# Kernel optimization log

Hardware: AMD Instinct MI355X
Metric: run time of the kernel (lower is better)

Reference implementation:

```python
import jax, jax.numpy as jnp
import numpy as np

EPS = 1e-5

def layer_norm(h, g, b):
    m = h.mean(-1, keepdims=True)
    v = ((h - m) ** 2).mean(-1, keepdims=True)
    return (h - m) * jax.lax.rsqrt(v + EPS) * g + b

def setup_inputs() -> dict:
    key = jax.random.key(0)
    ks = jax.random.split(key, 16)
    B, D, C, H, EH, L = 64, 20000, 16, 64, 128, 32
    s = lambda k, fan_in, shape: jax.random.normal(k, shape, jnp.float32) / np.sqrt(fan_in)
    return {
        "x": jax.random.normal(ks[0], (B, D), jnp.float32),
        "mask": jax.random.randint(ks[1], (B, D), 0, 2, jnp.int32),
        "feature_embedding": jax.random.normal(ks[2], (D, C), jnp.float32),
        # h_layer: Linear(1+C -> H), LN, ReLU, Linear(H -> C), LN, ReLU
        "W1": s(ks[3], 1 + C, (1 + C, H)), "b1": jnp.zeros((H,), jnp.float32),
        "g1": jnp.ones((H,), jnp.float32), "be1": jnp.zeros((H,), jnp.float32),
        "W2": s(ks[4], H, (H, C)), "b2": jnp.zeros((C,), jnp.float32),
        "g2": jnp.ones((C,), jnp.float32), "be2": jnp.zeros((C,), jnp.float32),
        # encoder_mlp (FCLayers, 2 layers, LayerNorm + ReLU each): C -> EH -> 2L
        "We1": s(ks[5], C, (C, EH)), "bb1": jnp.zeros((EH,), jnp.float32),
        "gg1": jnp.ones((EH,), jnp.float32), "bbe1": jnp.zeros((EH,), jnp.float32),
        "We2": s(ks[6], EH, (EH, 2 * L)), "bb2": jnp.zeros((2 * L,), jnp.float32),
        "gg2": jnp.ones((2 * L,), jnp.float32), "bbe2": jnp.zeros((2 * L,), jnp.float32),
    }

def reference(x, mask, feature_embedding, W1, b1, g1, be1, W2, b2, g2, be2,
              We1, bb1, gg1, bbe1, We2, bb2, gg2, bbe2):
    B, D = x.shape
    C = feature_embedding.shape[1]
    # per-feature point-net: h_layer runs row-wise, so we compute it densely
    # for all (b, d) and zero out unobserved entries before pooling —
    # identical math to the per-sample masked gather in the original.
    h_in = jnp.concatenate(
        [x[..., None], jnp.broadcast_to(feature_embedding, (B, D, C))], axis=-1
    )  # [B, D, 1+C]
    h = jax.nn.relu(layer_norm(h_in @ W1 + b1, g1, be1))   # [B, D, H]
    h = jax.nn.relu(layer_norm(h @ W2 + b2, g2, be2))      # [B, D, C]
    m = mask.astype(h.dtype)
    summed = jnp.einsum('bdc,bd->bc', h, m)                # masked sum pool
    num_obs = jnp.maximum(m.sum(axis=1, keepdims=True), 1.0)
    c = summed / num_obs                                   # pool_mode='mean'
    # encoder_mlp
    e = jax.nn.relu(layer_norm(c @ We1 + bb1, gg1, bbe1))
    e = jax.nn.relu(layer_norm(e @ We2 + bb2, gg2, bbe2))  # [B, 2*latent]
    mu, logvar = jnp.split(e, 2, axis=-1)
    return mu, logvar
```

## Files before the change

### kernel.cpp

```cpp
#include <hip/hip_runtime.h>
#include <hip/hip_bf16.h>

#define EPSF 1e-5f

namespace {
constexpr int B = 64, D = 20000, C = 16, H = 64, EH = 128, L = 32;
constexpr int CHUNK = 256;
constexpr int GX = 26;
constexpr int PB = 16;
}

typedef __attribute__((ext_vector_type(8))) short bf16x8;
typedef __attribute__((ext_vector_type(4))) float f32x4;

static __device__ __forceinline__ unsigned short f2bf(float f) {
    __hip_bfloat16 h = __float2bfloat16(f);
    return __builtin_bit_cast(unsigned short, h);
}
static __device__ __forceinline__ unsigned int packbf(float lo, float hi) {
    return ((unsigned int)f2bf(hi) << 16) | (unsigned int)f2bf(lo);
}

__global__ __launch_bounds__(1024) void k_prep(
    const int* __restrict__ mask, const float* __restrict__ fe,
    const float* __restrict__ W1, const float* __restrict__ b1,
    const float* __restrict__ W2,
    unsigned short* __restrict__ cd, int* __restrict__ cnt,
    unsigned short* __restrict__ febf,
    unsigned short* __restrict__ W1T, unsigned short* __restrict__ W2T)
{
    const int t = threadIdx.x;
    if (blockIdx.x < B) {
        const int b = blockIdx.x;
        const int lane = t & 63, wid = t >> 6;
        __shared__ int wc[16];
        const size_t bD = (size_t)b * D;
        constexpr int NIT = (D + 1023) / 1024;
        int mv = (t < D) ? mask[bD + t] : 0;
        int base = 0;
        for (int it = 0; it < NIT; ++it) {
            int mv_next = 0;
            const int dn = (it + 1) * 1024 + t;
            if (it + 1 < NIT && dn < D) mv_next = mask[bD + dn];
            const unsigned long long bal = __ballot(mv != 0);
            if (lane == 0) wc[wid] = __popcll(bal);
            __syncthreads();
            int woff = 0, tot = 0;
            #pragma unroll
            for (int k2 = 0; k2 < 16; ++k2) {
                const int c0 = wc[k2];
                tot += c0;
                if (k2 < wid) woff += c0;
            }
            if (mv) {
                const int d = it * 1024 + t;
                const int pre = __popcll(bal & ((1ull << lane) - 1ull));
                cd[bD + base + woff + pre] = (unsigned short)d;
            }
            base += tot;
            __syncthreads();
            mv = mv_next;
        }
        if (t == 0) cnt[b] = base;
    } else {
        const int pb = blockIdx.x - B;
        const int gtid = pb * 1024 + t;
        for (int u = gtid; u < (D * C) / 8; u += PB * 1024) {
            const float4 f0 = *(const float4*)(fe + (size_t)u * 8);
            const float4 f1 = *(const float4*)(fe + (size_t)u * 8 + 4);
            uint4 pk;
            pk.x = packbf(f0.x, f0.y); pk.y = packbf(f0.z, f0.w);
            pk.z = packbf(f1.x, f1.y); pk.w = packbf(f1.z, f1.w);
            *(uint4*)(febf + (size_t)u * 8) = pk;
        }
        if (pb == 0) {
            for (int e = t; e < H * 32; e += 1024) {
                const int h = e >> 5, kk = e & 31;
                float v = 0.f;
                if (kk < 16)       v = W1[(kk + 1) * H + h];
                else if (kk == 16) v = W1[h];
                else if (kk == 17) v = b1[h];
                W1T[e] = f2bf(v);
            }
        } else if (pb == 1) {
            for (int e = t; e < C * H; e += 1024) {
                const int c0 = e >> 6, hh = e & 63;
                W2T[e] = f2bf(W2[hh * C + c0]);
            }
        }
    }
}

__global__ __launch_bounds__(256, 4) void k_rows(
    const float* __restrict__ x, const unsigned short* __restrict__ cd,
    const int* __restrict__ cnt, const unsigned short* __restrict__ febf,
    const unsigned short* __restrict__ W1T, const unsigned short* __restrict__ W2T,
    const float* __restrict__ g1, const float* __restrict__ be1,
    const float* __restrict__ g2, const float* __restrict__ be2,
    const float* __restrict__ b2,
    float* __restrict__ part)
{
    const int b  = blockIdx.y;
    const int bx = blockIdx.x;
    const int n  = cnt[b];
    const int tid = threadIdx.x;
    const int w = tid >> 6, lane = tid & 63;
    const int g = lane >> 4, q = lane & 15;
    const size_t bD = (size_t)b * D;

    bf16x8 w1f[4];
    #pragma unroll
    for (int m = 0; m < 4; ++m)
        w1f[m] = *(const bf16x8*)(W1T + (16 * m + q) * 32 + 8 * g);
    bf16x8 w2f[2];
    #pragma unroll
    for (int ks = 0; ks < 2; ++ks)
        w2f[ks] = *(const bf16x8*)(W2T + q * 64 + 32 * ks + 8 * g);

    float4 g1v[4], be1v[4];
    #pragma unroll
    for (int m = 0; m < 4; ++m) {
        g1v[m]  = *(const float4*)(g1  + 16 * m + 4 * g);
        be1v[m] = *(const float4*)(be1 + 16 * m + 4 * g);
    }
    const float4 g2v  = *(const float4*)(g2  + 4 * g);
    const float4 be2v = *(const float4*)(be2 + 4 * g);
    const float4 b2v  = *(const float4*)(b2  + 4 * g);

    __shared__ __align__(16) unsigned short Rs[4][4][8][16][8];
    __shared__ float wsum[4][16];

    f32x4 acc = {0.f, 0.f, 0.f, 0.f};

    const int nch = (n + CHUNK - 1) / CHUNK;
    for (int j = bx; j < nch; j += GX) {
        const int cbase = j * CHUNK + w * 64;

        bf16x8 hb[4];
        #pragma unroll
        for (int it = 0; it < 4; ++it) {
            const int gb = cbase + it * 16;
            bf16x8 hv;
            #pragma unroll
            for (int e = 0; e < 8; ++e) hv[e] = 0;
            if (gb < n) {
                const int idx = gb + q;
                const bool v = idx < n;
                if (g < 2) {
                    int d = 0;
                    if (v) d = cd[bD + idx];
                    hv = *(const bf16x8*)(febf + (size_t)d * 16 + 8 * g);
                } else if (g == 2) {
                    float xv = 0.f;
                    if (v) { const int d = cd[bD + idx]; xv = x[bD + d]; }
                    hv[0] = (short)f2bf(xv);
                    hv[1] = (short)0x3F80;
                }
            }
            hb[it] = hv;
        }

        #pragma unroll
        for (int it = 0; it < 4; ++it) {
            const int gb = cbase + it * 16;
            if (gb >= n) continue;
            const f32x4 z = {0.f, 0.f, 0.f, 0.f};
            f32x4 t1a[4];
            #pragma unroll
            for (int m = 0; m < 4; ++m)
                t1a[m] = __builtin_amdgcn_mfma_f32_16x16x32_bf16(w1f[m], hb[it], z, 0, 0, 0);

            float s0 = 0.f, s1 = 0.f, q0 = 0.f, q1 = 0.f;
            #pragma unroll
            for (int m = 0; m < 4; ++m) {
                s0 += t1a[m][0] + t1a[m][1];
                s1 += t1a[m][2] + t1a[m][3];
                q0 = fmaf(t1a[m][0], t1a[m][0], fmaf(t1a[m][1], t1a[m][1], q0));
                q1 = fmaf(t1a[m][2], t1a[m][2], fmaf(t1a[m][3], t1a[m][3], q1));
            }
            float s = s0 + s1, sq = q0 + q1;
            s  += __shfl_xor(s, 16);  sq += __shfl_xor(sq, 16);
            s  += __shfl_xor(s, 32);  sq += __shfl_xor(sq, 32);
            const float mean1 = s * (1.f / H);
            const float var1  = fmaxf(sq * (1.f / H) - mean1 * mean1, 0.f);
            const float rstd1 = rsqrtf(var1 + EPSF);

            #pragma unroll
            for (int m = 0; m < 4; ++m) {
                const float v0 = fmaxf(fmaf((t1a[m][0] - mean1) * rstd1, g1v[m].x, be1v[m].x), 0.f);
                const float v1 = fmaxf(fmaf((t1a[m][1] - mean1) * rstd1, g1v[m].y, be1v[m].y), 0.f);
                const float v2 = fmaxf(fmaf((t1a[m][2] - mean1) * rstd1, g1v[m].z, be1v[m].z), 0.f);
                const float v3 = fmaxf(fmaf((t1a[m][3] - mean1) * rstd1, g1v[m].w, be1v[m].w), 0.f);
                uint2 pk = make_uint2(packbf(v0, v1), packbf(v2, v3));
                *(uint2*)&Rs[w][it][2 * m + (g >> 1)][q][4 * (g & 1)] = pk;
            }

            const bf16x8 rb0 = *(const bf16x8*)&Rs[w][it][g][q][0];
            const bf16x8 rb1 = *(const bf16x8*)&Rs[w][it][4 + g][q][0];
            f32x4 a2 = __builtin_amdgcn_mfma_f32_16x16x32_bf16(w2f[0], rb0, z, 0, 0, 0);
            a2 = __builtin_amdgcn_mfma_f32_16x16x32_bf16(w2f[1], rb1, a2, 0, 0, 0);
            a2[0] += b2v.x; a2[1] += b2v.y; a2[2] += b2v.z; a2[3] += b2v.w;

            float s2 = (a2[0] + a2[1]) + (a2[2] + a2[3]);
            float q2 = fmaf(a2[0], a2[0], fmaf(a2[1], a2[1],
                       fmaf(a2[2], a2[2], a2[3] * a2[3])));
            s2 += __shfl_xor(s2, 16);  q2 += __shfl_xor(q2, 16);
            s2 += __shfl_xor(s2, 32);  q2 += __shfl_xor(q2, 32);
            const float mean2 = s2 * (1.f / C);
            const float var2  = fmaxf(q2 * (1.f / C) - mean2 * mean2, 0.f);
            const float rstd2 = rsqrtf(var2 + EPSF);
            const float vm = (gb + q < n) ? 1.f : 0.f;
            acc[0] += fmaxf(fmaf((a2[0] - mean2) * rstd2, g2v.x, be2v.x), 0.f) * vm;
            acc[1] += fmaxf(fmaf((a2[1] - mean2) * rstd2, g2v.y, be2v.y), 0.f) * vm;
            acc[2] += fmaxf(fmaf((a2[2] - mean2) * rstd2, g2v.z, be2v.z), 0.f) * vm;
            acc[3] += fmaxf(fmaf((a2[3] - mean2) * rstd2, g2v.w, be2v.w), 0.f) * vm;
        }
    }

    #pragma unroll
    for (int off = 1; off < 16; off <<= 1) {
        #pragma unroll
        for (int r = 0; r < 4; ++r) acc[r] += __shfl_xor(acc[r], off);
    }
    if (q == 0)
        *(float4*)&wsum[w][4 * g] = make_float4(acc[0], acc[1], acc[2], acc[3]);
    __syncthreads();
    if (tid < C)
        part[((size_t)b * GX + bx) * C + tid] =
            wsum[0][tid] + wsum[1][tid] + wsum[2][tid] + wsum[3][tid];
}

__global__ __launch_bounds__(EH) void k_enc(
    const float* __restrict__ part, const int* __restrict__ cnt,
    const float* __restrict__ We1, const float* __restrict__ bb1,
    const float* __restrict__ gg1, const float* __restrict__ bbe1,
    const float* __restrict__ We2, const float* __restrict__ bb2,
    const float* __restrict__ gg2, const float* __restrict__ bbe2,
    float* __restrict__ out)
{
    const int b = blockIdx.x;
    const int t = threadIdx.x;
    __shared__ float cc[C];
    __shared__ float stats[2];
    __shared__ float buf[EH];
    __shared__ float buf2[2 * L];

    const int n = cnt[b];
    if (t < C) {
        float s = 0.f;
        #pragma unroll
        for (int j = 0; j < GX; ++j)
            s += part[((size_t)b * GX + j) * C + t];
        cc[t] = s;
    }
    __syncthreads();
    const float inv = 1.f / fmaxf((float)n, 1.f);

    float v1 = bb1[t];
    #pragma unroll
    for (int c = 0; c < C; ++c)
        v1 = fmaf(cc[c] * inv, We1[c * EH + t], v1);
    buf[t] = v1;
    __syncthreads();
    if (t == 0) {
        float s = 0.f, ss = 0.f;
        for (int j2 = 0; j2 < EH; ++j2) { s += buf[j2]; ss = fmaf(buf[j2], buf[j2], ss); }
        float mn = s * (1.f / EH);
        float vr = fmaxf(ss * (1.f / EH) - mn * mn, 0.f);
        stats[0] = mn; stats[1] = rsqrtf(vr + EPSF);
    }
    __syncthreads();
    float e1 = fmaxf(fmaf((v1 - stats[0]) * stats[1], gg1[t], bbe1[t]), 0.f);
    __syncthreads();
    buf[t] = e1;
    __syncthreads();

    float v2 = 0.f;
    if (t < 2 * L) {
        v2 = bb2[t];
        #pragma unroll
        for (int h = 0; h < EH; ++h)
            v2 = fmaf(buf[h], We2[h * (2 * L) + t], v2);
        buf2[t] = v2;
    }
    __syncthreads();
    if (t == 0) {
        float s = 0.f, ss = 0.f;
        for (int j2 = 0; j2 < 2 * L; ++j2) { s += buf2[j2]; ss = fmaf(buf2[j2], buf2[j2], ss); }
        float mn = s * (1.f / (2 * L));
        float vr = fmaxf(ss * (1.f / (2 * L)) - mn * mn, 0.f);
        stats[0] = mn; stats[1] = rsqrtf(vr + EPSF);
    }
    __syncthreads();
    if (t < 2 * L) {
        float e2 = fmaxf(fmaf((v2 - stats[0]) * stats[1], gg2[t], bbe2[t]), 0.f);
        if (t < L) out[(size_t)b * L + t]                       = e2;
        else       out[(size_t)B * L + (size_t)b * L + (t - L)] = e2;
    }
}

extern "C" void kernel_launch(void* const* d_in, const int* in_sizes, int n_in,
                              void* d_out, int out_size, void* d_ws, size_t ws_size,
                              hipStream_t stream) {
    const float* x    = (const float*)d_in[0];
    const int*   mask = (const int*)d_in[1];
    const float* fe   = (const float*)d_in[2];
    const float* W1   = (const float*)d_in[3];
    const float* b1   = (const float*)d_in[4];
    const float* g1   = (const float*)d_in[5];
    const float* be1  = (const float*)d_in[6];
    const float* W2   = (const float*)d_in[7];
    const float* b2   = (const float*)d_in[8];
    const float* g2   = (const float*)d_in[9];
    const float* be2  = (const float*)d_in[10];
    const float* We1  = (const float*)d_in[11];
    const float* bb1  = (const float*)d_in[12];
    const float* gg1  = (const float*)d_in[13];
    const float* bbe1 = (const float*)d_in[14];
    const float* We2  = (const float*)d_in[15];
    const float* bb2  = (const float*)d_in[16];
    const float* gg2  = (const float*)d_in[17];
    const float* bbe2 = (const float*)d_in[18];
    float* out = (float*)d_out;

    char* wp = (char*)d_ws;
    float* part     = (float*)wp;               wp += (size_t)B * GX * C * 4;
    int*   cnt      = (int*)wp;                 wp += (size_t)B * 4;
    unsigned short* W1T  = (unsigned short*)wp; wp += (size_t)H * 32 * 2;
    unsigned short* W2T  = (unsigned short*)wp; wp += (size_t)C * H * 2;
    unsigned short* febf = (unsigned short*)wp; wp += (size_t)D * C * 2;
    unsigned short* cd   = (unsigned short*)wp;

    hipLaunchKernelGGL(k_prep, dim3(B + PB), dim3(1024), 0, stream,
                       mask, fe, W1, b1, W2, cd, cnt, febf, W1T, W2T);
    hipLaunchKernelGGL(k_rows, dim3(GX, B), dim3(256), 0, stream,
                       x, cd, cnt, febf, W1T, W2T, g1, be1, g2, be2, b2, part);
    hipLaunchKernelGGL(k_enc, dim3(B), dim3(EH), 0, stream,
                       part, cnt, We1, bb1, gg1, bbe1, We2, bb2, gg2, bbe2, out);
}
```

Measured before the change: 54.73 us.

## Flatten row work into global 64-row units and pass layer-1 output in registers

The row kernel stops using a fixed grid of 26 blocks per batch. Each wave now takes a global 64-element unit found through a prefix sum of per-batch unit counts, which balances load across batches with different observed counts. W1T rows are permuted so the first MFMA's output layout matches the second MFMA's input operand layout, so the shared-memory round trip and the block-level reduction go away. Each wave does one cooperative index load plus lane shuffles instead of per-lane index loads. In exchange, every unit writes its own partial row, so the encoder kernel gets a prefix scan and a strided reduction over a much larger partial buffer.

```diff
diff --git a/kernel.cpp b/kernel.cpp
--- a/kernel.cpp
+++ b/kernel.cpp
@@ -5,13 +5,14 @@
 
 namespace {
 constexpr int B = 64, D = 20000, C = 16, H = 64, EH = 128, L = 32;
-constexpr int CHUNK = 256;
-constexpr int GX = 26;
 constexpr int PB = 16;
+constexpr int NB = 1024;
+constexpr int MAXU = B * ((D + 63) / 64);
 }
 
 typedef __attribute__((ext_vector_type(8))) short bf16x8;
 typedef __attribute__((ext_vector_type(4))) float f32x4;
+typedef __attribute__((ext_vector_type(4))) unsigned int u32x4;
 
 static __device__ __forceinline__ unsigned short f2bf(float f) {
     __hip_bfloat16 h = __float2bfloat16(f);
@@ -75,7 +76,9 @@
         }
         if (pb == 0) {
             for (int e = t; e < H * 32; e += 1024) {
-                const int h = e >> 5, kk = e & 31;
+                const int rIdx = e >> 5, kk = e & 31;
+                const int m = rIdx >> 4, rho = rIdx & 15;
+                const int h = 32 * (m >> 1) + 8 * (rho >> 2) + 4 * (m & 1) + (rho & 3);
                 float v = 0.f;
                 if (kk < 16)       v = W1[(kk + 1) * H + h];
                 else if (kk == 16) v = W1[h];
@@ -100,13 +103,19 @@
     const float* __restrict__ b2,
     float* __restrict__ part)
 {
-    const int b  = blockIdx.y;
-    const int bx = blockIdx.x;
-    const int n  = cnt[b];
     const int tid = threadIdx.x;
     const int w = tid >> 6, lane = tid & 63;
     const int g = lane >> 4, q = lane & 15;
-    const size_t bD = (size_t)b * D;
+
+    const int cv  = cnt[lane];
+    const int nuv = (cv + 63) >> 6;
+    int Pi = nuv;
+    #pragma unroll
+    for (int off = 1; off < 64; off <<= 1) {
+        const int pv = __shfl_up(Pi, off);
+        if (lane >= off) Pi += pv;
+    }
+    const int T = __shfl(Pi, 63);
 
     bf16x8 w1f[4];
     #pragma unroll
@@ -120,51 +129,50 @@
     float4 g1v[4], be1v[4];
     #pragma unroll
     for (int m = 0; m < 4; ++m) {
-        g1v[m]  = *(const float4*)(g1  + 16 * m + 4 * g);
-        be1v[m] = *(const float4*)(be1 + 16 * m + 4 * g);
+        const int h0 = 32 * (m >> 1) + 8 * g + 4 * (m & 1);
+        g1v[m]  = *(const float4*)(g1  + h0);
+        be1v[m] = *(const float4*)(be1 + h0);
     }
     const float4 g2v  = *(const float4*)(g2  + 4 * g);
     const float4 be2v = *(const float4*)(be2 + 4 * g);
     const float4 b2v  = *(const float4*)(b2  + 4 * g);
 
-    __shared__ __align__(16) unsigned short Rs[4][4][8][16][8];
-    __shared__ float wsum[4][16];
-
-    f32x4 acc = {0.f, 0.f, 0.f, 0.f};
-
-    const int nch = (n + CHUNK - 1) / CHUNK;
-    for (int j = bx; j < nch; j += GX) {
-        const int cbase = j * CHUNK + w * 64;
+    const f32x4 z = {0.f, 0.f, 0.f, 0.f};
+
+    for (int u = blockIdx.x * 4 + w; u < T; u += NB * 4) {
+        const unsigned long long bl = __ballot(Pi <= u);
+        const int b   = __popcll(bl);
+        const int Pb  = __shfl(Pi, b);
+        const int nub = __shfl(nuv, b);
+        const int n   = __shfl(cv, b);
+        const int base = (u - (Pb - nub)) * 64;
+        const size_t bD = (size_t)b * D;
+
+        const int idx  = base + lane;
+        const int craw = (int)cd[bD + idx];
+        const int dv   = (idx < n) ? craw : 0;
 
         bf16x8 hb[4];
         #pragma unroll
         for (int it = 0; it < 4; ++it) {
-            const int gb = cbase + it * 16;
+            const int dd = __shfl(dv, (it << 4) + q);
             bf16x8 hv;
             #pragma unroll
             for (int e = 0; e < 8; ++e) hv[e] = 0;
-            if (gb < n) {
-                const int idx = gb + q;
-                const bool v = idx < n;
-                if (g < 2) {
-                    int d = 0;
-                    if (v) d = cd[bD + idx];
-                    hv = *(const bf16x8*)(febf + (size_t)d * 16 + 8 * g);
-                } else if (g == 2) {
-                    float xv = 0.f;
-                    if (v) { const int d = cd[bD + idx]; xv = x[bD + d]; }
-                    hv[0] = (short)f2bf(xv);
-                    hv[1] = (short)0x3F80;
-                }
+            if (g < 2) {
+                hv = *(const bf16x8*)(febf + (size_t)dd * 16 + 8 * g);
+            } else if (g == 2) {
+                hv[0] = (short)f2bf(x[bD + dd]);
+                hv[1] = (short)0x3F80;
             }
             hb[it] = hv;
         }
 
+        f32x4 lacc = {0.f, 0.f, 0.f, 0.f};
         #pragma unroll
         for (int it = 0; it < 4; ++it) {
-            const int gb = cbase + it * 16;
+            const int gb = base + (it << 4);
             if (gb >= n) continue;
-            const f32x4 z = {0.f, 0.f, 0.f, 0.f};
             f32x4 t1a[4];
             #pragma unroll
             for (int m = 0; m < 4; ++m)
@@ -185,18 +193,21 @@
             const float var1  = fmaxf(sq * (1.f / H) - mean1 * mean1, 0.f);
             const float rstd1 = rsqrtf(var1 + EPSF);
 
+            unsigned int pw[8];
             #pragma unroll
             for (int m = 0; m < 4; ++m) {
                 const float v0 = fmaxf(fmaf((t1a[m][0] - mean1) * rstd1, g1v[m].x, be1v[m].x), 0.f);
                 const float v1 = fmaxf(fmaf((t1a[m][1] - mean1) * rstd1, g1v[m].y, be1v[m].y), 0.f);
                 const float v2 = fmaxf(fmaf((t1a[m][2] - mean1) * rstd1, g1v[m].z, be1v[m].z), 0.f);
                 const float v3 = fmaxf(fmaf((t1a[m][3] - mean1) * rstd1, g1v[m].w, be1v[m].w), 0.f);
-                uint2 pk = make_uint2(packbf(v0, v1), packbf(v2, v3));
-                *(uint2*)&Rs[w][it][2 * m + (g >> 1)][q][4 * (g & 1)] = pk;
-            }
-
-            const bf16x8 rb0 = *(const bf16x8*)&Rs[w][it][g][q][0];
-            const bf16x8 rb1 = *(const bf16x8*)&Rs[w][it][4 + g][q][0];
+                pw[2 * m]     = packbf(v0, v1);
+                pw[2 * m + 1] = packbf(v2, v3);
+            }
+            const u32x4 r0 = {pw[0], pw[1], pw[2], pw[3]};
+            const u32x4 r1 = {pw[4], pw[5], pw[6], pw[7]};
+            const bf16x8 rb0 = __builtin_bit_cast(bf16x8, r0);
+            const bf16x8 rb1 = __builtin_bit_cast(bf16x8, r1);
+
             f32x4 a2 = __builtin_amdgcn_mfma_f32_16x16x32_bf16(w2f[0], rb0, z, 0, 0, 0);
             a2 = __builtin_amdgcn_mfma_f32_16x16x32_bf16(w2f[1], rb1, a2, 0, 0, 0);
             a2[0] += b2v.x; a2[1] += b2v.y; a2[2] += b2v.z; a2[3] += b2v.w;
@@ -210,24 +221,21 @@
             const float var2  = fmaxf(q2 * (1.f / C) - mean2 * mean2, 0.f);
             const float rstd2 = rsqrtf(var2 + EPSF);
             const float vm = (gb + q < n) ? 1.f : 0.f;
-            acc[0] += fmaxf(fmaf((a2[0] - mean2) * rstd2, g2v.x, be2v.x), 0.f) * vm;
-            acc[1] += fmaxf(fmaf((a2[1] - mean2) * rstd2, g2v.y, be2v.y), 0.f) * vm;
-            acc[2] += fmaxf(fmaf((a2[2] - mean2) * rstd2, g2v.z, be2v.z), 0.f) * vm;
-            acc[3] += fmaxf(fmaf((a2[3] - mean2) * rstd2, g2v.w, be2v.w), 0.f) * vm;
-        }
-    }
-
-    #pragma unroll
-    for (int off = 1; off < 16; off <<= 1) {
-        #pragma unroll
-        for (int r = 0; r < 4; ++r) acc[r] += __shfl_xor(acc[r], off);
-    }
-    if (q == 0)
-        *(float4*)&wsum[w][4 * g] = make_float4(acc[0], acc[1], acc[2], acc[3]);
-    __syncthreads();
-    if (tid < C)
-        part[((size_t)b * GX + bx) * C + tid] =
-            wsum[0][tid] + wsum[1][tid] + wsum[2][tid] + wsum[3][tid];
+            lacc[0] += fmaxf(fmaf((a2[0] - mean2) * rstd2, g2v.x, be2v.x), 0.f) * vm;
+            lacc[1] += fmaxf(fmaf((a2[1] - mean2) * rstd2, g2v.y, be2v.y), 0.f) * vm;
+            lacc[2] += fmaxf(fmaf((a2[2] - mean2) * rstd2, g2v.z, be2v.z), 0.f) * vm;
+            lacc[3] += fmaxf(fmaf((a2[3] - mean2) * rstd2, g2v.w, be2v.w), 0.f) * vm;
+        }
+
+        #pragma unroll
+        for (int off = 1; off < 16; off <<= 1) {
+            #pragma unroll
+            for (int r = 0; r < 4; ++r) lacc[r] += __shfl_xor(lacc[r], off);
+        }
+        if (q == 0)
+            *(float4*)(part + (size_t)u * C + 4 * g) =
+                make_float4(lacc[0], lacc[1], lacc[2], lacc[3]);
+    }
 }
 
 __global__ __launch_bounds__(EH) void k_enc(
@@ -240,18 +248,40 @@
 {
     const int b = blockIdx.x;
     const int t = threadIdx.x;
+    __shared__ int sP[64];
+    __shared__ float red[8][16];
     __shared__ float cc[C];
     __shared__ float stats[2];
     __shared__ float buf[EH];
     __shared__ float buf2[2 * L];
 
+    if (t < 64) {
+        int p = (cnt[t] + 63) >> 6;
+        #pragma unroll
+        for (int off = 1; off < 64; off <<= 1) {
+            const int pv = __shfl_up(p, off);
+            if (t >= off) p += pv;
+        }
+        sP[t] = p;
+    }
+    __syncthreads();
     const int n = cnt[b];
+    const int row0 = (b == 0) ? 0 : sP[b - 1];
+    const int rows = sP[b] - row0;
+
+    {
+        const int c = t & 15, s = t >> 4;
+        float ps = 0.f;
+        for (int r = s; r < rows; r += 8)
+            ps += part[(size_t)(row0 + r) * C + c];
+        red[s][c] = ps;
+    }
+    __syncthreads();
     if (t < C) {
-        float s = 0.f;
-        #pragma unroll
-        for (int j = 0; j < GX; ++j)
-            s += part[((size_t)b * GX + j) * C + t];
-        cc[t] = s;
+        float v = 0.f;
+        #pragma unroll
+        for (int s = 0; s < 8; ++s) v += red[s][t];
+        cc[t] = v;
     }
     __syncthreads();
     const float inv = 1.f / fmaxf((float)n, 1.f);
@@ -324,7 +354,7 @@
     float* out = (float*)d_out;
 
     char* wp = (char*)d_ws;
-    float* part     = (float*)wp;               wp += (size_t)B * GX * C * 4;
+    float* part     = (float*)wp;               wp += (size_t)MAXU * C * 4;
     int*   cnt      = (int*)wp;                 wp += (size_t)B * 4;
     unsigned short* W1T  = (unsigned short*)wp; wp += (size_t)H * 32 * 2;
     unsigned short* W2T  = (unsigned short*)wp; wp += (size_t)C * H * 2;
@@ -333,7 +363,7 @@
 
     hipLaunchKernelGGL(k_prep, dim3(B + PB), dim3(1024), 0, stream,
                        mask, fe, W1, b1, W2, cd, cnt, febf, W1T, W2T);
-    hipLaunchKernelGGL(k_rows, dim3(GX, B), dim3(256), 0, stream,
+    hipLaunchKernelGGL(k_rows, dim3(NB), dim3(256), 0, stream,
                        x, cd, cnt, febf, W1T, W2T, g1, be1, g2, be2, b2, part);
     hipLaunchKernelGGL(k_enc, dim3(B), dim3(EH), 0, stream,
                        part, cnt, We1, bb1, gg1, bbe1, We2, bb2, gg2, bbe2, out);
```

Result: faster. 52.79 us (-3.5%).
